# Kernel tuning notes

Measured on AMD Instinct MI355X. Metric: run time of the kernel, lower is better.

The kernel has to match this reference:

```python
import jax, jax.numpy as jnp
import numpy as np

B, T, D, H, K, V, W = 2, 2048, 768, 12, 64, 64, 1024
EPS = 1e-6


def setup_inputs() -> dict:
    key = jax.random.key(0)
    ks = jax.random.split(key, 10)
    std = 0.02
    return {
        "x": jax.random.normal(ks[0], (B, T, D), jnp.float32),
        "gdn_state": jax.random.normal(ks[1], (B, H, K, V), jnp.float32),
        "Wq": jax.random.normal(ks[2], (D, H * K), jnp.float32) * std,
        "Wk": jax.random.normal(ks[3], (D, H * K), jnp.float32) * std,
        "Wv": jax.random.normal(ks[4], (D, H * K), jnp.float32) * std,
        "Wo": jax.random.normal(ks[5], (H * K, D), jnp.float32) * std,
        "Wgq": jax.random.normal(ks[6], (D, H * K), jnp.float32) * std,
        "Wro": jax.random.normal(ks[7], (H * V, D), jnp.float32) * std,
        "Wg": jax.random.normal(ks[8], (D, H), jnp.float32) * std,
        "bg": jnp.full((H,), 1.0, jnp.float32),  # swa_gate_init
        "norm_w": jnp.ones((D,), jnp.float32),
    }


def reference(x, gdn_state, Wq, Wk, Wv, Wo, Wgq, Wro, Wg, bg, norm_w):
    # RMSNorm
    xn = x * jax.lax.rsqrt(jnp.mean(x * x, axis=-1, keepdims=True) + EPS) * norm_w

    def proj(w):  # (B,T,D)@(D,HK) -> (B,H,T,K)
        return (xn @ w).reshape(B, T, H, K).transpose(0, 2, 1, 3)

    q, k, v = proj(Wq), proj(Wk), proj(Wv)
    scale = K ** -0.5

    scores = jnp.einsum("bhqk,bhsk->bhqs", q, k) * scale  # (B,H,T,T)
    i = jnp.arange(T)[:, None]
    j = jnp.arange(T)[None, :]
    allowed = (j <= i) & (j >= i - W)  # causal sliding window
    scores = jnp.where(allowed, scores, -jnp.inf)
    attn = jax.nn.softmax(scores, axis=-1)

    local = jnp.einsum("bhqs,bhsk->bhqk", attn, v)
    local = local.transpose(0, 2, 1, 3).reshape(B, T, H * K) @ Wo  # (B,T,D)

    # GDN state retrieval
    qg = jax.nn.relu((xn @ Wgq).reshape(B, T, H, K).transpose(0, 2, 1, 3))  # (B,H,T,K)
    retrieved = jnp.einsum("bhkv,bhtk->bhtv", gdn_state, qg)  # (B,H,T,V)
    retrieval = retrieved.transpose(0, 2, 1, 3).reshape(B, T, H * V) @ Wro  # (B,T,D)
    gate = jax.nn.sigmoid(xn @ Wg + bg)  # (B,T,H)
    retrieval = jnp.mean(gate, axis=-1, keepdims=True) * retrieval

    return x + local + retrieval
```

## Files before the change

### kernel.cpp

```cpp
#include <hip/hip_runtime.h>
#include <math.h>
#include <stdint.h>

typedef float f32x4 __attribute__((ext_vector_type(4)));
typedef __bf16 bf16x8 __attribute__((ext_vector_type(8)));
typedef __bf16 bf16x4 __attribute__((ext_vector_type(4)));

constexpr int Bc = 2, Tc = 2048, Dc = 768, Hc = 12, Wc = 1024;
#define CEXP 0.18033688011112042f

__device__ __forceinline__ f32x4 mfma_bf16(bf16x8 a, bf16x8 b, f32x4 c) {
    return __builtin_amdgcn_mfma_f32_16x16x32_bf16(a, b, c, 0, 0, 0);
}
__device__ __forceinline__ void gload16(const void* g, void* l) {
    __builtin_amdgcn_global_load_lds(
        (const __attribute__((address_space(1))) uint32_t*)g,
        (__attribute__((address_space(3))) uint32_t*)l, 16, 0, 0);
}
__device__ __forceinline__ uint32_t pack2(float a, float b) {
    union { __bf16 h[2]; uint32_t u; } x;
    x.h[0] = (__bf16)a; x.h[1] = (__bf16)b; return x.u;
}
__device__ __forceinline__ void s_wait_vm4() { asm volatile("s_waitcnt vmcnt(4)" ::: "memory"); }
__device__ __forceinline__ void s_wait_vm2() { asm volatile("s_waitcnt vmcnt(2)" ::: "memory"); }
__device__ __forceinline__ void s_wait_vm0() { asm volatile("s_waitcnt vmcnt(0)" ::: "memory"); }
__device__ __forceinline__ void s_wait_lgkm0() { asm volatile("s_waitcnt lgkmcnt(0)" ::: "memory"); }
__device__ __forceinline__ void bar()        { __builtin_amdgcn_s_barrier(); }
__device__ __forceinline__ void wait_tiles2(int infl) {
    if (infl >= 2) s_wait_vm4();
    else if (infl == 1) s_wait_vm2();
    else s_wait_vm0();
}

__global__ __launch_bounds__(256) void k_prep_w(
    const float* __restrict__ Wq, const float* __restrict__ Wk,
    const float* __restrict__ Wv, const float* __restrict__ Wgq,
    const float* __restrict__ Wo, const float* __restrict__ Wro,
    __bf16* __restrict__ wTproj, __bf16* __restrict__ wTout)
{
    __shared__ __bf16 ldsT[64][66];
    const int wsel = blockIdx.y;
    const float* srcs[6] = {Wq, Wk, Wv, Wgq, Wo, Wro};
    const float* src = srcs[wsel];
    __bf16* dst; int dstride, koff;
    if (wsel < 4) { dst = wTproj + (size_t)wsel * Dc * Dc; dstride = Dc;  koff = 0; }
    else if (wsel == 4) { dst = wTout; dstride = 1536; koff = 0; }
    else { dst = wTout; dstride = 1536; koff = 768; }
    const float scale = (wsel == 0) ? CEXP : 1.0f;

    int tile = blockIdx.x;
    int tk = tile % 12, tn = tile / 12;
    int k0 = tk * 64, n0 = tn * 64;
    int i = threadIdx.x, rsub = i >> 4, c4 = i & 15;
#pragma unroll
    for (int rep = 0; rep < 4; ++rep) {
        int row = rep * 16 + rsub;
        float4 v = *(const float4*)(src + (size_t)(k0 + row) * Dc + n0 + c4 * 4);
        ldsT[c4 * 4 + 0][row] = (__bf16)(v.x * scale);
        ldsT[c4 * 4 + 1][row] = (__bf16)(v.y * scale);
        ldsT[c4 * 4 + 2][row] = (__bf16)(v.z * scale);
        ldsT[c4 * 4 + 3][row] = (__bf16)(v.w * scale);
    }
    __syncthreads();
#pragma unroll
    for (int rep = 0; rep < 4; ++rep) {
        int n = rep * 16 + rsub;
        bf16x4 o = *(const bf16x4*)&ldsT[n][c4 * 4];
        *(bf16x4*)(dst + (size_t)(n0 + n) * dstride + koff + k0 + c4 * 4) = o;
    }
}

__global__ __launch_bounds__(256) void k_prep_state(
    const float* __restrict__ st, __bf16* __restrict__ stT)
{
    int idx = blockIdx.x * 256 + threadIdx.x;
    int bh = idx >> 12, kk = (idx >> 6) & 63, vv = idx & 63;
    stT[(size_t)bh * 4096 + vv * 64 + kk] = (__bf16)st[idx];
}

__global__ __launch_bounds__(256) void k_prep_wgt(
    const float* __restrict__ Wg, float* __restrict__ WgT)
{
    int i = blockIdx.x * 256 + threadIdx.x;
    int h = i / Dc, d = i - h * Dc;
    WgT[i] = Wg[d * 12 + h];
}

__global__ __launch_bounds__(256) void k_rmsnorm(
    const float* __restrict__ x, const float* __restrict__ norm_w,
    __bf16* __restrict__ xnb)
{
    int row = blockIdx.x, tid = threadIdx.x;
    const float* xr = x + (size_t)row * Dc;
    float4 v = make_float4(0.f, 0.f, 0.f, 0.f);
    float ss = 0.f;
    if (tid < 192) {
        v = ((const float4*)xr)[tid];
        ss = v.x * v.x + v.y * v.y + v.z * v.z + v.w * v.w;
    }
#pragma unroll
    for (int m = 32; m; m >>= 1) ss += __shfl_xor(ss, m, 64);
    __shared__ float red[4];
    if ((tid & 63) == 0) red[tid >> 6] = ss;
    __syncthreads();
    float tot = red[0] + red[1] + red[2] + red[3];
    float rms = rsqrtf(tot * (1.f / 768.f) + 1e-6f);
    if (tid < 192) {
        float4 nw = ((const float4*)norm_w)[tid];
        bf16x4 o;
        o[0] = (__bf16)(v.x * rms * nw.x);
        o[1] = (__bf16)(v.y * rms * nw.y);
        o[2] = (__bf16)(v.z * rms * nw.z);
        o[3] = (__bf16)(v.w * rms * nw.w);
        *(bf16x4*)(xnb + (size_t)row * Dc + tid * 4) = o;
    }
}

__global__ __launch_bounds__(256) void k_gate(
    const __bf16* __restrict__ xnb, const float* __restrict__ WgT,
    const float* __restrict__ bg, float* __restrict__ gmean)
{
    int row = blockIdx.x * 4 + (threadIdx.x >> 6);
    int lane = threadIdx.x & 63;
    const __bf16* xr = xnb + (size_t)row * Dc;
    float p[12];
#pragma unroll
    for (int h = 0; h < 12; ++h) p[h] = 0.f;
    for (int d = lane; d < Dc; d += 64) {
        float xv = (float)xr[d];
#pragma unroll
        for (int h = 0; h < 12; ++h) p[h] += xv * WgT[h * Dc + d];
    }
#pragma unroll
    for (int h = 0; h < 12; ++h) {
#pragma unroll
        for (int m = 32; m; m >>= 1) p[h] += __shfl_xor(p[h], m, 64);
    }
    if (lane == 0) {
        float s = 0.f;
#pragma unroll
        for (int h = 0; h < 12; ++h) s += 1.f / (1.f + expf(-(p[h] + bg[h])));
        gmean[row] = s * (1.f / 12.f);
    }
}

template <int MODE>
__global__ __launch_bounds__(256) void k_gemm(
    const __bf16* __restrict__ A, const __bf16* __restrict__ BT,
    const float* __restrict__ xres, float* __restrict__ outf,
    __bf16* __restrict__ qb, __bf16* __restrict__ kbf,
    __bf16* __restrict__ vtb, __bf16* __restrict__ qgb)
{
    constexpr int BM = (MODE == 0) ? 128 : 64;
    constexpr int BN = (MODE == 0) ? 128 : 64;
    constexpr int KD = (MODE == 0) ? 768 : 1536;
    constexpr int BK = (MODE == 0) ? 32 : 64;
    constexpr int KI = BK / 32;
    constexpr int WM = BM / 2, WN = BN / 2;
    constexpr int MI = WM / 16, NI = WN / 16;
    constexpr int NK = KD / BK;
    constexpr int GR = BK / 8;
    constexpr int ACH = BM * BK / 2048;
    constexpr int BCH = BN * BK / 2048;
    __shared__ __bf16 As[2][BM * BK];
    __shared__ __bf16 Bs[2][BN * BK];
    const int tid = threadIdx.x, w = tid >> 6, lane = tid & 63;
    const int g = lane >> 4, t = lane & 15;
    int id = blockIdx.x, xcd = id & 7, l = id >> 3;
    int m0, n0;
    if (MODE == 0) {
        m0 = (((xcd & 3) * 8) + (l & 7)) * BM;
        n0 = (((xcd >> 2) * 12) + (l >> 3)) * BN;
    } else {
        m0 = ((xcd * 8) + (l & 7)) * BM;
        n0 = (l >> 3) * BN;
    }
    const __bf16* Abase = A + (size_t)m0 * KD;
    const __bf16* Bbase = BT + (size_t)n0 * KD;
    const int wrow = (w >> 1) * WM, wcol = (w & 1) * WN;

    auto STAGE = [&](int buf, int k0) {
#pragma unroll
        for (int c = 0; c < ACH; ++c) {
            int chunk = c * 256 + tid, row = chunk / GR, cix = chunk % GR;
            gload16(Abase + (size_t)row * KD + k0 + cix * 8, &As[buf][chunk * 8]);
        }
#pragma unroll
        for (int c = 0; c < BCH; ++c) {
            int chunk = c * 256 + tid, row = chunk / GR, cix = chunk % GR;
            gload16(Bbase + (size_t)row * KD + k0 + cix * 8, &Bs[buf][chunk * 8]);
        }
    };

    f32x4 acc[MI][NI] = {};
    STAGE(0, 0);
    STAGE(1, BK);
    for (int ks = 0; ks < NK; ++ks) {
        if (ks == NK - 1) s_wait_vm0(); else s_wait_vm4();
        bar();
        const __bf16* Ab = As[ks & 1];
        const __bf16* Bb = Bs[ks & 1];
        bf16x8 af[MI][KI], bfr[NI][KI];
#pragma unroll
        for (int kk = 0; kk < KI; ++kk) {
#pragma unroll
            for (int mi = 0; mi < MI; ++mi)
                af[mi][kk] = *(const bf16x8*)(Ab + (wrow + mi * 16 + t) * BK + kk * 32 + g * 8);
#pragma unroll
            for (int ni = 0; ni < NI; ++ni)
                bfr[ni][kk] = *(const bf16x8*)(Bb + (wcol + ni * 16 + t) * BK + kk * 32 + g * 8);
        }
        s_wait_lgkm0();
        __builtin_amdgcn_sched_barrier(0);
        bar();
        if (ks + 2 < NK) STAGE(ks & 1, (ks + 2) * BK);
        __builtin_amdgcn_s_setprio(1);
#pragma unroll
        for (int kk = 0; kk < KI; ++kk)
#pragma unroll
            for (int mi = 0; mi < MI; ++mi)
#pragma unroll
                for (int ni = 0; ni < NI; ++ni)
                    acc[mi][ni] = mfma_bf16(af[mi][kk], bfr[ni][kk], acc[mi][ni]);
        __builtin_amdgcn_s_setprio(0);
    }
    const int region = (MODE == 0) ? (n0 / 768) : 0;
    if (MODE == 0 && region == 2) {
#pragma unroll
        for (int mi = 0; mi < MI; ++mi)
#pragma unroll
            for (int ni = 0; ni < NI; ++ni) {
                int grow0 = m0 + wrow + mi * 16 + g * 4;
                int b = grow0 >> 11, ti0 = grow0 & (Tc - 1);
                int c = (n0 + wcol + ni * 16 + t) - 1536;
                int h = c >> 6, kd = c & 63;
                int kap = ti0 & 63;
                int rho = (kap & 32) | (((kap >> 2) & 3) << 3) | (((kap >> 4) & 1) << 2);
                int ts = (ti0 & ~63) | (rho ^ ((kd & 7) << 3));
                bf16x4 o;
                o[0] = (__bf16)acc[mi][ni][0]; o[1] = (__bf16)acc[mi][ni][1];
                o[2] = (__bf16)acc[mi][ni][2]; o[3] = (__bf16)acc[mi][ni][3];
                *(bf16x4*)(vtb + ((size_t)(b * Hc + h) * 64 + kd) * Tc + ts) = o;
            }
    } else {
#pragma unroll
        for (int mi = 0; mi < MI; ++mi)
#pragma unroll
            for (int ni = 0; ni < NI; ++ni)
#pragma unroll
                for (int r = 0; r < 4; ++r) {
                    int grow = m0 + wrow + mi * 16 + g * 4 + r;
                    int gcol = n0 + wcol + ni * 16 + t;
                    float v = acc[mi][ni][r];
                    if (MODE == 1) {
                        size_t idx = (size_t)grow * Dc + gcol;
                        outf[idx] = xres[idx] + v;
                    } else {
                        int c = gcol - region * 768;
                        int h = c >> 6, kd = c & 63;
                        int b = grow >> 11, ti = grow & (Tc - 1);
                        if (region == 0)
                            qb[((size_t)(b * Hc + h) * Tc + ti) * 64 + kd] = (__bf16)v;
                        else if (region == 1) {
                            int kds = kd ^ ((ti & 7) << 3);
                            kbf[((size_t)(b * Hc + h) * Tc + ti) * 64 + kds] = (__bf16)v;
                        } else
                            qgb[((size_t)(b * Hc + h) * Tc + ti) * 64 + kd] = (__bf16)fmaxf(v, 0.f);
                    }
                }
    }
}

__global__ __launch_bounds__(512, 6) void k_attn(
    const __bf16* __restrict__ q, const __bf16* __restrict__ k,
    const __bf16* __restrict__ vt, const __bf16* __restrict__ qg,
    const __bf16* __restrict__ stateT, const float* __restrict__ gmean,
    __bf16* __restrict__ ac)
{
    __shared__ __bf16 Ks[3][64 * 64];
    __shared__ __bf16 Vs[3][64 * 64];
    int id = blockIdx.x, xcd = id & 7, l = id >> 3;
    int nid = xcd * 96 + l;
    int sblk = nid & 31, h = (nid >> 5) % Hc, b = nid / (32 * Hc);
    int tid = threadIdx.x;
    int w = tid >> 6, lane = tid & 63;
    int g = lane >> 4, t = lane & 15;
    int q0 = sblk * 64, qw = q0 + (w & 3) * 16;
    const int myPar = w >> 2;
    const __bf16* qb = q + (size_t)(b * Hc + h) * Tc * 64;
    const __bf16* kb = k + (size_t)(b * Hc + h) * Tc * 64;
    const __bf16* vb = vt + (size_t)(b * Hc + h) * 64 * Tc;

    bf16x8 qf0 = *(const bf16x8*)(qb + (size_t)(qw + t) * 64 + g * 8);
    bf16x8 qf1 = *(const bf16x8*)(qb + (size_t)(qw + t) * 64 + 32 + g * 8);

    const int qi = qw + t;
    const int lowB = qi - Wc;
    const int xr = t & 7;

    f32x4 oacc[4] = {};
    float lsum = 0.f;

    const int s_begin = (q0 >= Wc) ? q0 - Wc : 0;
    const int NT = (q0 + 64 - s_begin) >> 6;

    auto STAGE = [&](int buf, int s0) {
        int ch = tid;
        gload16(kb + (size_t)(s0 + (ch >> 3)) * 64 + (ch & 7) * 8, &Ks[buf][ch * 8]);
        gload16(vb + (size_t)(ch >> 3) * Tc + s0 + (ch & 7) * 8, &Vs[buf][ch * 8]);
    };

    STAGE(0, s_begin);
    if (NT > 1) STAGE(1, s_begin + 64);
    if (NT > 2) STAGE(2, s_begin + 128);
    int buf = 0;
    for (int it = 0; it < NT; ++it) {
        int s0 = s_begin + it * 64;
        wait_tiles2(NT - 1 - it);
        bar();
        if ((it & 1) == myPar) {
            const __bf16* Kt = Ks[buf];
            const __bf16* Vt = Vs[buf];
            f32x4 sc[4];
            __builtin_amdgcn_s_setprio(1);
#pragma unroll
            for (int sub = 0; sub < 4; ++sub) {
                const __bf16* kr = Kt + (sub * 16 + t) * 64;
                bf16x8 kA = *(const bf16x8*)(kr + ((g ^ xr) << 3));
                bf16x8 kB = *(const bf16x8*)(kr + (((g + 4) ^ xr) << 3));
                f32x4 s = {};
                s = mfma_bf16(kA, qf0, s);
                s = mfma_bf16(kB, qf1, s);
                sc[sub] = s;
            }
            __builtin_amdgcn_s_setprio(0);
            float pv[4][4];
#pragma unroll
            for (int sub = 0; sub < 4; ++sub)
#pragma unroll
                for (int r = 0; r < 4; ++r) {
                    int kk = s0 + sub * 16 + g * 4 + r;
                    float e = exp2f(sc[sub][r]);
                    float val = (kk <= qi && kk >= lowB) ? e : 0.f;
                    pv[sub][r] = val;
                    lsum += val;
                }
            __builtin_amdgcn_s_setprio(1);
#pragma unroll
            for (int ks = 0; ks < 2; ++ks) {
                union { uint32_t u[4]; bf16x8 v; } pf;
                pf.u[0] = pack2(pv[ks * 2][0], pv[ks * 2][1]);
                pf.u[1] = pack2(pv[ks * 2][2], pv[ks * 2][3]);
                pf.u[2] = pack2(pv[ks * 2 + 1][0], pv[ks * 2 + 1][1]);
                pf.u[3] = pack2(pv[ks * 2 + 1][2], pv[ks * 2 + 1][3]);
#pragma unroll
                for (int n = 0; n < 4; ++n) {
                    const __bf16* vrow = Vt + (n * 16 + t) * 64;
                    bf16x8 vf = *(const bf16x8*)(vrow + ((((ks * 4) + g) ^ xr) << 3));
                    oacc[n] = mfma_bf16(pf.v, vf, oacc[n]);
                }
            }
            __builtin_amdgcn_s_setprio(0);
        }
        s_wait_lgkm0();
        __builtin_amdgcn_sched_barrier(0);
        bar();
        if (it + 3 < NT) STAGE(buf, s0 + 192);
        buf = (buf == 2) ? 0 : buf + 1;
    }
    float* cb = (float*)&Ks[0][0];
    if (w >= 4) {
        float* dst = cb + ((size_t)((w - 4) * 64 + lane)) * 20;
#pragma unroll
        for (int n = 0; n < 4; ++n) *(f32x4*)(dst + n * 4) = oacc[n];
        dst[16] = lsum;
    }
    bar();
    if (w < 4) {
        const float* src = cb + ((size_t)(w * 64 + lane)) * 20;
#pragma unroll
        for (int n = 0; n < 4; ++n) oacc[n] += *(const f32x4*)(src + n * 4);
        lsum += src[16];
        lsum += __shfl_xor(lsum, 16, 64);
        lsum += __shfl_xor(lsum, 32, 64);
        float linv = 1.f / lsum;
        float lq[4];
#pragma unroll
        for (int r = 0; r < 4; ++r) lq[r] = __shfl(linv, g * 4 + r, 64);
#pragma unroll
        for (int n = 0; n < 4; ++n)
#pragma unroll
            for (int r = 0; r < 4; ++r) {
                int qrow = qw + g * 4 + r;
                ac[(size_t)(b * Tc + qrow) * 1536 + h * 64 + n * 16 + t] =
                    (__bf16)(oacc[n][r] * lq[r]);
            }
        const __bf16* qgp = qg + (size_t)(b * Hc + h) * Tc * 64;
        const __bf16* sb = stateT + (size_t)(b * Hc + h) * 4096;
        bf16x8 a0 = *(const bf16x8*)(qgp + (size_t)(qw + t) * 64 + g * 8);
        bf16x8 a1 = *(const bf16x8*)(qgp + (size_t)(qw + t) * 64 + 32 + g * 8);
#pragma unroll
        for (int n = 0; n < 4; ++n) {
            bf16x8 b0 = *(const bf16x8*)(sb + (n * 16 + t) * 64 + g * 8);
            bf16x8 b1 = *(const bf16x8*)(sb + (n * 16 + t) * 64 + 32 + g * 8);
            f32x4 acc2 = {};
            acc2 = mfma_bf16(a0, b0, acc2);
            acc2 = mfma_bf16(a1, b1, acc2);
#pragma unroll
            for (int r = 0; r < 4; ++r) {
                int ti = qw + g * 4 + r;
                float gm = gmean[b * Tc + ti];
                ac[(size_t)(b * Tc + ti) * 1536 + 768 + h * 64 + n * 16 + t] =
                    (__bf16)(acc2[r] * gm);
            }
        }
    }
}

extern "C" void kernel_launch(void* const* d_in, const int* in_sizes, int n_in,
                              void* d_out, int out_size, void* d_ws, size_t ws_size,
                              hipStream_t stream) {
    (void)in_sizes; (void)n_in; (void)out_size; (void)ws_size;
    const float* x     = (const float*)d_in[0];
    const float* gdn   = (const float*)d_in[1];
    const float* Wq    = (const float*)d_in[2];
    const float* Wk    = (const float*)d_in[3];
    const float* Wv    = (const float*)d_in[4];
    const float* Wo    = (const float*)d_in[5];
    const float* Wgq   = (const float*)d_in[6];
    const float* Wro   = (const float*)d_in[7];
    const float* Wg    = (const float*)d_in[8];
    const float* bg    = (const float*)d_in[9];
    const float* normw = (const float*)d_in[10];
    float* out = (float*)d_out;

    char* p = (char*)d_ws;
    auto alloc = [&](size_t bytes) -> char* {
        char* r = p; p += (bytes + 255) & ~(size_t)255; return r;
    };
    constexpr size_t NROW = (size_t)Bc * Tc;
    __bf16* xnb    = (__bf16*)alloc(NROW * Dc * 2);
    __bf16* wTproj = (__bf16*)alloc((size_t)4 * Dc * Dc * 2);
    __bf16* wTout  = (__bf16*)alloc((size_t)Dc * 1536 * 2);
    __bf16* stT    = (__bf16*)alloc((size_t)Bc * Hc * 64 * 64 * 2);
    __bf16* qbuf   = (__bf16*)alloc(NROW * Dc * 2);
    __bf16* kbuf   = (__bf16*)alloc(NROW * Dc * 2);
    __bf16* qgbuf  = (__bf16*)alloc(NROW * Dc * 2);
    __bf16* vtbuf  = (__bf16*)alloc(NROW * Dc * 2);
    __bf16* ac     = (__bf16*)alloc(NROW * 1536 * 2);
    float*  gmean  = (float*)alloc(NROW * 4);
    float*  WgT    = (float*)alloc((size_t)12 * Dc * 4);

    k_prep_w<<<dim3(144, 6), 256, 0, stream>>>(Wq, Wk, Wv, Wgq, Wo, Wro, wTproj, wTout);
    k_prep_state<<<(Bc * Hc * 64 * 64) / 256, 256, 0, stream>>>(gdn, stT);
    k_prep_wgt<<<36, 256, 0, stream>>>(Wg, WgT);
    k_rmsnorm<<<NROW, 256, 0, stream>>>(x, normw, xnb);
    k_gate<<<NROW / 4, 256, 0, stream>>>(xnb, WgT, bg, gmean);

    k_gemm<0><<<768, 256, 0, stream>>>(xnb, wTproj, nullptr, nullptr,
                                       qbuf, kbuf, vtbuf, qgbuf);
    k_attn<<<768, 512, 0, stream>>>(qbuf, kbuf, vtbuf, qgbuf, stT, gmean, ac);
    k_gemm<1><<<768, 256, 0, stream>>>(ac, wTout, x, out,
                                       nullptr, nullptr, nullptr, nullptr);
}
```

Baseline: 117.6 us.

## Process two 64-row query tiles per attention block to reuse K/V tiles

Each attention block now covers 128 query rows instead of 64, with every wave holding two 16-row query fragments (A and B) that share each staged K/V tile from LDS. The grid halves to 384 blocks and launch bounds drop to 4 waves-per-EU occupancy to make room for the doubled accumulators. This halves K/V global and LDS traffic per query and fuses the softmax and pack into the score loop. In exchange it raises register pressure, lowers parallelism, and adds extra fully-masked tiles on the causal edge, so wave occupancy and load balance may suffer.

```diff
diff --git a/kernel.cpp b/kernel.cpp
--- a/kernel.cpp
+++ b/kernel.cpp
@@ -271,7 +271,7 @@
     }
 }
 
-__global__ __launch_bounds__(512, 6) void k_attn(
+__global__ __launch_bounds__(512, 4) void k_attn(
     const __bf16* __restrict__ q, const __bf16* __restrict__ k,
     const __bf16* __restrict__ vt, const __bf16* __restrict__ qg,
     const __bf16* __restrict__ stateT, const float* __restrict__ gmean,
@@ -280,29 +280,32 @@
     __shared__ __bf16 Ks[3][64 * 64];
     __shared__ __bf16 Vs[3][64 * 64];
     int id = blockIdx.x, xcd = id & 7, l = id >> 3;
-    int nid = xcd * 96 + l;
-    int sblk = nid & 31, h = (nid >> 5) % Hc, b = nid / (32 * Hc);
+    int nid = xcd * 48 + l;
+    int sblk = nid & 15, h = (nid >> 4) % Hc, b = nid / 192;
     int tid = threadIdx.x;
     int w = tid >> 6, lane = tid & 63;
     int g = lane >> 4, t = lane & 15;
-    int q0 = sblk * 64, qw = q0 + (w & 3) * 16;
-    const int myPar = w >> 2;
+    int q0 = sblk * 128;
+    int wq = w & 3, p = w >> 2;
+    int qwA = q0 + wq * 16, qwB = qwA + 64;
     const __bf16* qb = q + (size_t)(b * Hc + h) * Tc * 64;
     const __bf16* kb = k + (size_t)(b * Hc + h) * Tc * 64;
     const __bf16* vb = vt + (size_t)(b * Hc + h) * 64 * Tc;
 
-    bf16x8 qf0 = *(const bf16x8*)(qb + (size_t)(qw + t) * 64 + g * 8);
-    bf16x8 qf1 = *(const bf16x8*)(qb + (size_t)(qw + t) * 64 + 32 + g * 8);
-
-    const int qi = qw + t;
-    const int lowB = qi - Wc;
+    bf16x8 qfA0 = *(const bf16x8*)(qb + (size_t)(qwA + t) * 64 + g * 8);
+    bf16x8 qfA1 = *(const bf16x8*)(qb + (size_t)(qwA + t) * 64 + 32 + g * 8);
+    bf16x8 qfB0 = *(const bf16x8*)(qb + (size_t)(qwB + t) * 64 + g * 8);
+    bf16x8 qfB1 = *(const bf16x8*)(qb + (size_t)(qwB + t) * 64 + 32 + g * 8);
+
+    const int qiA = qwA + t, qiB = qwB + t;
+    const int loA = qiA - Wc, loB = qiB - Wc;
     const int xr = t & 7;
 
-    f32x4 oacc[4] = {};
-    float lsum = 0.f;
+    f32x4 oaccA[4] = {}, oaccB[4] = {};
+    float lsumA = 0.f, lsumB = 0.f;
 
     const int s_begin = (q0 >= Wc) ? q0 - Wc : 0;
-    const int NT = (q0 + 64 - s_begin) >> 6;
+    const int NT = (q0 + 128 - s_begin) >> 6;
 
     auto STAGE = [&](int buf, int s0) {
         int ch = tid;
@@ -318,46 +321,48 @@
         int s0 = s_begin + it * 64;
         wait_tiles2(NT - 1 - it);
         bar();
-        if ((it & 1) == myPar) {
+        if ((it & 1) == p) {
             const __bf16* Kt = Ks[buf];
             const __bf16* Vt = Vs[buf];
-            f32x4 sc[4];
+            uint32_t pfA[8], pfB[8];
             __builtin_amdgcn_s_setprio(1);
 #pragma unroll
             for (int sub = 0; sub < 4; ++sub) {
                 const __bf16* kr = Kt + (sub * 16 + t) * 64;
                 bf16x8 kA = *(const bf16x8*)(kr + ((g ^ xr) << 3));
                 bf16x8 kB = *(const bf16x8*)(kr + (((g + 4) ^ xr) << 3));
-                f32x4 s = {};
-                s = mfma_bf16(kA, qf0, s);
-                s = mfma_bf16(kB, qf1, s);
-                sc[sub] = s;
-            }
-            __builtin_amdgcn_s_setprio(0);
-            float pv[4][4];
-#pragma unroll
-            for (int sub = 0; sub < 4; ++sub)
+                f32x4 sA = {}, sB = {};
+                sA = mfma_bf16(kA, qfA0, sA);
+                sA = mfma_bf16(kB, qfA1, sA);
+                sB = mfma_bf16(kA, qfB0, sB);
+                sB = mfma_bf16(kB, qfB1, sB);
+                float vA[4], vB[4];
 #pragma unroll
                 for (int r = 0; r < 4; ++r) {
                     int kk = s0 + sub * 16 + g * 4 + r;
-                    float e = exp2f(sc[sub][r]);
-                    float val = (kk <= qi && kk >= lowB) ? e : 0.f;
-                    pv[sub][r] = val;
-                    lsum += val;
+                    float eA = exp2f(sA[r]);
+                    float eB = exp2f(sB[r]);
+                    vA[r] = (kk <= qiA && kk >= loA) ? eA : 0.f;
+                    vB[r] = (kk <= qiB && kk >= loB) ? eB : 0.f;
+                    lsumA += vA[r];
+                    lsumB += vB[r];
                 }
-            __builtin_amdgcn_s_setprio(1);
+                pfA[sub * 2 + 0] = pack2(vA[0], vA[1]);
+                pfA[sub * 2 + 1] = pack2(vA[2], vA[3]);
+                pfB[sub * 2 + 0] = pack2(vB[0], vB[1]);
+                pfB[sub * 2 + 1] = pack2(vB[2], vB[3]);
+            }
 #pragma unroll
             for (int ks = 0; ks < 2; ++ks) {
-                union { uint32_t u[4]; bf16x8 v; } pf;
-                pf.u[0] = pack2(pv[ks * 2][0], pv[ks * 2][1]);
-                pf.u[1] = pack2(pv[ks * 2][2], pv[ks * 2][3]);
-                pf.u[2] = pack2(pv[ks * 2 + 1][0], pv[ks * 2 + 1][1]);
-                pf.u[3] = pack2(pv[ks * 2 + 1][2], pv[ks * 2 + 1][3]);
+                union { uint32_t u[4]; bf16x8 v; } pA, pB;
+#pragma unroll
+                for (int j = 0; j < 4; ++j) { pA.u[j] = pfA[ks * 4 + j]; pB.u[j] = pfB[ks * 4 + j]; }
 #pragma unroll
                 for (int n = 0; n < 4; ++n) {
                     const __bf16* vrow = Vt + (n * 16 + t) * 64;
                     bf16x8 vf = *(const bf16x8*)(vrow + ((((ks * 4) + g) ^ xr) << 3));
-                    oacc[n] = mfma_bf16(pf.v, vf, oacc[n]);
+                    oaccA[n] = mfma_bf16(pA.v, vf, oaccA[n]);
+                    oaccB[n] = mfma_bf16(pB.v, vf, oaccB[n]);
                 }
             }
             __builtin_amdgcn_s_setprio(0);
@@ -368,50 +373,58 @@
         if (it + 3 < NT) STAGE(buf, s0 + 192);
         buf = (buf == 2) ? 0 : buf + 1;
     }
-    float* cb = (float*)&Ks[0][0];
-    if (w >= 4) {
-        float* dst = cb + ((size_t)((w - 4) * 64 + lane)) * 20;
-#pragma unroll
-        for (int n = 0; n < 4; ++n) *(f32x4*)(dst + n * 4) = oacc[n];
-        dst[16] = lsum;
+    float* cbA = (float*)&Ks[0][0];
+    float* cbB = (float*)&Vs[0][0];
+    if (p == 1) {
+        float* dA = cbA + ((size_t)(wq * 64 + lane)) * 20;
+        float* dB = cbB + ((size_t)(wq * 64 + lane)) * 20;
+#pragma unroll
+        for (int n = 0; n < 4; ++n) { *(f32x4*)(dA + n * 4) = oaccA[n]; *(f32x4*)(dB + n * 4) = oaccB[n]; }
+        dA[16] = lsumA; dB[16] = lsumB;
     }
     bar();
-    if (w < 4) {
-        const float* src = cb + ((size_t)(w * 64 + lane)) * 20;
-#pragma unroll
-        for (int n = 0; n < 4; ++n) oacc[n] += *(const f32x4*)(src + n * 4);
-        lsum += src[16];
-        lsum += __shfl_xor(lsum, 16, 64);
-        lsum += __shfl_xor(lsum, 32, 64);
-        float linv = 1.f / lsum;
-        float lq[4];
-#pragma unroll
-        for (int r = 0; r < 4; ++r) lq[r] = __shfl(linv, g * 4 + r, 64);
+    if (p == 0) {
+        const float* sA = cbA + ((size_t)(wq * 64 + lane)) * 20;
+        const float* sB = cbB + ((size_t)(wq * 64 + lane)) * 20;
+#pragma unroll
+        for (int n = 0; n < 4; ++n) { oaccA[n] += *(const f32x4*)(sA + n * 4); oaccB[n] += *(const f32x4*)(sB + n * 4); }
+        lsumA += sA[16]; lsumB += sB[16];
+        lsumA += __shfl_xor(lsumA, 16, 64); lsumA += __shfl_xor(lsumA, 32, 64);
+        lsumB += __shfl_xor(lsumB, 16, 64); lsumB += __shfl_xor(lsumB, 32, 64);
+        float liA = 1.f / lsumA, liB = 1.f / lsumB;
+        float lqA[4], lqB[4];
+#pragma unroll
+        for (int r = 0; r < 4; ++r) { lqA[r] = __shfl(liA, g * 4 + r, 64); lqB[r] = __shfl(liB, g * 4 + r, 64); }
 #pragma unroll
         for (int n = 0; n < 4; ++n)
 #pragma unroll
             for (int r = 0; r < 4; ++r) {
-                int qrow = qw + g * 4 + r;
-                ac[(size_t)(b * Tc + qrow) * 1536 + h * 64 + n * 16 + t] =
-                    (__bf16)(oacc[n][r] * lq[r]);
+                int qrA = qwA + g * 4 + r, qrB = qwB + g * 4 + r;
+                ac[(size_t)(b * Tc + qrA) * 1536 + h * 64 + n * 16 + t] =
+                    (__bf16)(oaccA[n][r] * lqA[r]);
+                ac[(size_t)(b * Tc + qrB) * 1536 + h * 64 + n * 16 + t] =
+                    (__bf16)(oaccB[n][r] * lqB[r]);
             }
         const __bf16* qgp = qg + (size_t)(b * Hc + h) * Tc * 64;
         const __bf16* sb = stateT + (size_t)(b * Hc + h) * 4096;
-        bf16x8 a0 = *(const bf16x8*)(qgp + (size_t)(qw + t) * 64 + g * 8);
-        bf16x8 a1 = *(const bf16x8*)(qgp + (size_t)(qw + t) * 64 + 32 + g * 8);
+        bf16x8 aA0 = *(const bf16x8*)(qgp + (size_t)(qwA + t) * 64 + g * 8);
+        bf16x8 aA1 = *(const bf16x8*)(qgp + (size_t)(qwA + t) * 64 + 32 + g * 8);
+        bf16x8 aB0 = *(const bf16x8*)(qgp + (size_t)(qwB + t) * 64 + g * 8);
+        bf16x8 aB1 = *(const bf16x8*)(qgp + (size_t)(qwB + t) * 64 + 32 + g * 8);
 #pragma unroll
         for (int n = 0; n < 4; ++n) {
             bf16x8 b0 = *(const bf16x8*)(sb + (n * 16 + t) * 64 + g * 8);
             bf16x8 b1 = *(const bf16x8*)(sb + (n * 16 + t) * 64 + 32 + g * 8);
-            f32x4 acc2 = {};
-            acc2 = mfma_bf16(a0, b0, acc2);
-            acc2 = mfma_bf16(a1, b1, acc2);
+            f32x4 rA = {}, rB = {};
+            rA = mfma_bf16(aA0, b0, rA); rA = mfma_bf16(aA1, b1, rA);
+            rB = mfma_bf16(aB0, b0, rB); rB = mfma_bf16(aB1, b1, rB);
 #pragma unroll
             for (int r = 0; r < 4; ++r) {
-                int ti = qw + g * 4 + r;
-                float gm = gmean[b * Tc + ti];
-                ac[(size_t)(b * Tc + ti) * 1536 + 768 + h * 64 + n * 16 + t] =
-                    (__bf16)(acc2[r] * gm);
+                int tA = qwA + g * 4 + r, tB = qwB + g * 4 + r;
+                ac[(size_t)(b * Tc + tA) * 1536 + 768 + h * 64 + n * 16 + t] =
+                    (__bf16)(rA[r] * gmean[b * Tc + tA]);
+                ac[(size_t)(b * Tc + tB) * 1536 + 768 + h * 64 + n * 16 + t] =
+                    (__bf16)(rB[r] * gmean[b * Tc + tB]);
             }
         }
     }
@@ -459,7 +472,7 @@
 
     k_gemm<0><<<768, 256, 0, stream>>>(xnb, wTproj, nullptr, nullptr,
                                        qbuf, kbuf, vtbuf, qgbuf);
-    k_attn<<<768, 512, 0, stream>>>(qbuf, kbuf, vtbuf, qgbuf, stT, gmean, ac);
+    k_attn<<<384, 512, 0, stream>>>(qbuf, kbuf, vtbuf, qgbuf, stT, gmean, ac);
     k_gemm<1><<<768, 256, 0, stream>>>(ac, wTout, x, out,
                                        nullptr, nullptr, nullptr, nullptr);
 }
```

New measurement: 130.3 us. 1.11x slower.
